# Kernel tuning notes

Measured on AMD Instinct MI355X. Metric: run time of the kernel, lower is better.

## Reference

```python
import jax, jax.numpy as jnp
import numpy as np

N = 50000
E = 800000
IN_DIM = 128
HID = 32
HEADS = 8
OUT_DIM = 2
NEG_SLOPE = 0.2


def setup_inputs() -> dict:
    key = jax.random.key(0)
    ks = jax.random.split(key, 10)
    x = jax.random.normal(ks[0], (N, IN_DIM), dtype=jnp.float32)
    edge_index = jax.random.randint(ks[1], (2, E), 0, N, dtype=jnp.int64)
    s = 0.1
    W1 = jax.random.normal(ks[2], (IN_DIM, HEADS * HID), dtype=jnp.float32) * s
    att_src1 = jax.random.normal(ks[3], (HEADS, HID), dtype=jnp.float32) * s
    att_dst1 = jax.random.normal(ks[4], (HEADS, HID), dtype=jnp.float32) * s
    b1 = jnp.zeros((HEADS * HID,), dtype=jnp.float32)
    W2 = jax.random.normal(ks[5], (HEADS * HID, OUT_DIM), dtype=jnp.float32) * s
    att_src2 = jax.random.normal(ks[6], (1, OUT_DIM), dtype=jnp.float32) * s
    att_dst2 = jax.random.normal(ks[7], (1, OUT_DIM), dtype=jnp.float32) * s
    b2 = jnp.zeros((OUT_DIM,), dtype=jnp.float32)
    return {"x": x, "edge_index": edge_index, "W1": W1, "att_src1": att_src1,
            "att_dst1": att_dst1, "b1": b1, "W2": W2, "att_src2": att_src2,
            "att_dst2": att_dst2, "b2": b2}


def gat_conv(x, src, dst, W, att_src, att_dst, bias, concat):
    # PyG GATConv (add_self_loops handled by caller already appended in src/dst)
    H, C = att_src.shape
    n = x.shape[0]
    h = (x @ W).reshape(n, H, C)                       # [N,H,C]
    a_src = jnp.einsum('nhc,hc->nh', h, att_src)       # [N,H]
    a_dst = jnp.einsum('nhc,hc->nh', h, att_dst)       # [N,H]
    e = jax.nn.leaky_relu(a_src[src] + a_dst[dst], NEG_SLOPE)  # [Etot,H]
    m = jax.lax.stop_gradient(jax.ops.segment_max(e, dst, num_segments=n))
    ee = jnp.exp(e - m[dst])
    denom = jax.ops.segment_sum(ee, dst, num_segments=n)
    alpha = ee / denom[dst]                            # segment softmax over incoming edges
    out = jax.ops.segment_sum(alpha[:, :, None] * h[src], dst, num_segments=n)  # [N,H,C]
    if concat:
        out = out.reshape(n, H * C)
    else:
        out = out.mean(axis=1)
    return out + bias


def reference(x, edge_index, W1, att_src1, att_dst1, b1, W2, att_src2, att_dst2, b2):
    n = x.shape[0]
    loop = jnp.arange(n, dtype=edge_index.dtype)
    src = jnp.concatenate([edge_index[0], loop])
    dst = jnp.concatenate([edge_index[1], loop])
    h = gat_conv(x, src, dst, W1, att_src1, att_dst1, b1, concat=True)
    h = jax.nn.elu(h)
    # dropout inactive in eval mode
    h = gat_conv(h, src, dst, W2, att_src2, att_dst2, b2, concat=False)
    return jax.nn.log_softmax(h, axis=1)
```

## Files before the change

kernel.cpp:

```cpp
#include <hip/hip_runtime.h>
#include <hip/hip_bf16.h>

#define NEG_SLOPE 0.2f
#define BSTRIDE 6144

typedef float f32x4 __attribute__((ext_vector_type(4)));
typedef short s16x4 __attribute__((ext_vector_type(4)));
typedef short bf16x8 __attribute__((ext_vector_type(8)));

__device__ __forceinline__ float lrelu(float x) { return x > 0.f ? x : NEG_SLOPE * x; }
__device__ __forceinline__ float bf2f(unsigned u) {
    return __uint_as_float(u << 16);
}
__device__ __forceinline__ unsigned short f2bf(float f) {
    unsigned int u = __float_as_uint(f);
    return (unsigned short)((u + 0x7FFF + ((u >> 16) & 1)) >> 16);
}

__device__ __forceinline__ int load_src(const int* ei, int E, int e, int is64) {
    return is64 ? ei[2 * (size_t)e] : ei[e];
}
__device__ __forceinline__ int load_dst(const int* ei, int E, int e, int is64) {
    return is64 ? ei[2 * (size_t)E + 2 * (size_t)e] : ei[(size_t)E + e];
}

__global__ void init2_kernel(const int* __restrict__ ei, int* __restrict__ flag,
                             int* __restrict__ bktCur) {
    int t = threadIdx.x;
    bktCur[t] = t * BSTRIDE;
    if (t == 0) {
        int z = 1;
        for (int k = 0; k < 64; ++k) if (ei[2 * k + 1] != 0) { z = 0; break; }
        *flag = z;
    }
}

__global__ __launch_bounds__(256) void bin_scatter(const int* __restrict__ ei, int E, int n,
                                                   const int* __restrict__ flag,
                                                   int* __restrict__ bktCur,
                                                   int* __restrict__ binned) {
    __shared__ int hist[256];
    __shared__ int gb[256];
    int t = threadIdx.x;
    hist[t] = 0;
    __syncthreads();
    int is64 = *flag;
    int base = blockIdx.x * 2048;
    int Etot = E + n;
    int rec[8], rb[8], rr[8];
#pragma unroll
    for (int k = 0; k < 8; ++k) {
        int e = base + k * 256 + t;
        rb[k] = -1;
        if (e < Etot) {
            int s, d;
            if (e < E) { s = load_src(ei, E, e, is64); d = load_dst(ei, E, e, is64); }
            else       { s = d = e - E; }
            int b = d >> 8;
            rb[k] = b;
            rec[k] = s | ((d & 255) << 24);
            rr[k] = atomicAdd(&hist[b], 1);
        }
    }
    __syncthreads();
    if (hist[t]) gb[t] = atomicAdd(&bktCur[t], hist[t]);
    __syncthreads();
#pragma unroll
    for (int k = 0; k < 8; ++k)
        if (rb[k] >= 0) binned[gb[rb[k]] + rr[k]] = rec[k];
}

__global__ __launch_bounds__(256) void bucket_build(const int* __restrict__ bktCur,
                                                    const int* __restrict__ binned,
                                                    int* __restrict__ offs,
                                                    int* __restrict__ degOut,
                                                    int* __restrict__ csr, int n) {
    __shared__ int deg[256];
    __shared__ int sd[256];
    int b = blockIdx.x;
    int t = threadIdx.x;
    int lo = b * BSTRIDE, hi = bktCur[b];
    deg[t] = 0;
    __syncthreads();
    for (int i = lo + t; i < hi; i += 256)
        atomicAdd(&deg[((unsigned)binned[i]) >> 24], 1);
    __syncthreads();
    int v = deg[t];
    sd[t] = v;
    __syncthreads();
    for (int o = 1; o < 256; o <<= 1) {
        int x = (t >= o) ? sd[t - o] : 0;
        __syncthreads();
        sd[t] += x;
        __syncthreads();
    }
    int excl = lo + sd[t] - v;
    int node = (b << 8) + t;
    if (node < n) { offs[node] = excl; degOut[node] = v; }
    __syncthreads();
    deg[t] = excl;
    __syncthreads();
    for (int i = lo + t; i < hi; i += 256) {
        unsigned r = (unsigned)binned[i];
        int pos = atomicAdd(&deg[r >> 24], 1);
        csr[pos] = (int)(r & 0xFFFFFF);
    }
}

__global__ __launch_bounds__(256) void w1prep_kernel(
        const float* __restrict__ W1, const float* __restrict__ att_src1,
        const float* __restrict__ att_dst1, unsigned short* __restrict__ w1t) {
    int t = threadIdx.x;
    if (blockIdx.x < 128) {
        int v = blockIdx.x * 256 + t;
        int col = v & 255, k = v >> 8;
        w1t[(size_t)col * 128 + k] = f2bf(W1[(size_t)k * 256 + col]);
    } else {
#pragma unroll
        for (int i = 0; i < 8; ++i) {
            int v = t + 256 * i;
            int j = v & 15, k = v >> 4;
            const float* av = (j < 8) ? att_src1 : att_dst1;
            int h = j & 7;
            float s = 0.f;
            for (int c = 0; c < 32; ++c)
                s += W1[(size_t)k * 256 + 32 * h + c] * av[h * 32 + c];
            w1t[(size_t)(256 + j) * 128 + k] = f2bf(s);
        }
    }
}

__device__ __forceinline__ bf16x8 read_frag(const char* base, int row, int kb) {
    int swz = (row & 7) << 4;
    const char* p = base + row * 256;
    s16x4 lo = *(const s16x4*)(p + (kb ^ swz));
    s16x4 hi = *(const s16x4*)(p + ((kb + 32) ^ swz));
    return __builtin_shufflevector(lo, hi, 0, 1, 2, 3, 4, 5, 6, 7);
}

__device__ __forceinline__ void load_px(const float* __restrict__ x, int m0, int n, int t,
                                        f32x4 (&px)[2][4]) {
#pragma unroll
    for (int q = 0; q < 2; ++q) {
        int u = t + 256 * q;
        int row = u >> 3, kseg = u & 7;
        int gr = m0 + row;
        bool ok = (u < 384) && (gr < n);
        const f32x4* p = (const f32x4*)(x + (size_t)gr * 128 + kseg * 16);
#pragma unroll
        for (int j = 0; j < 4; ++j) {
            f32x4 z = {0.f, 0.f, 0.f, 0.f};
            px[q][j] = ok ? p[j] : z;
        }
    }
}

#define XOFF 69632
__global__ __launch_bounds__(256, 2) void gemm1_kernel(
        const float* __restrict__ x, const unsigned short* __restrict__ w1t,
        unsigned short* __restrict__ h1u, float* __restrict__ asrc1,
        float* __restrict__ adst1, int n, int nchunk) {
    __shared__ __align__(16) char lds[81920];
    const int t = threadIdx.x;
    const int lane = t & 63, w = t >> 6;
    const int l15 = lane & 15, g = lane >> 4;

    for (int u = t; u < 4352; u += 256) {
        int col = u >> 4, seg = u & 15;
        int4 v = *(const int4*)(w1t + (size_t)col * 128 + seg * 8);
        *(int4*)(lds + col * 256 + ((seg * 16) ^ ((col & 7) << 4))) = v;
    }

    int c0 = blockIdx.x * 2;
    f32x4 px[2][4];
    load_px(x, c0 * 48, n, t, px);
    __syncthreads();

    bf16x8 Bf[4][5];
#pragma unroll
    for (int ks = 0; ks < 4; ++ks) {
#pragma unroll
        for (int nt = 0; nt < 5; ++nt) {
            if (nt < 4 || w == 0) {
                int col = (nt < 4) ? (64 * w + 16 * nt + l15) : (256 + l15);
                Bf[ks][nt] = read_frag(lds, col, 64 * ks + 8 * g);
            }
        }
    }

    for (int cc = 0; cc < 2; ++cc) {
        int chunk = c0 + cc;
        if (chunk >= nchunk) break;
        int m0 = chunk * 48;
#pragma unroll
        for (int q = 0; q < 2; ++q) {
            int u = t + 256 * q;
            if (u < 384) {
                int row = u >> 3, kseg = u & 7;
                union { unsigned short us[16]; int4 v[2]; } pk;
#pragma unroll
                for (int j = 0; j < 4; ++j)
#pragma unroll
                    for (int e = 0; e < 4; ++e) pk.us[j * 4 + e] = f2bf(px[q][j][e]);
                int base = XOFF + row * 256;
                int swz = (row & 7) << 4;
                *(int4*)(lds + base + ((kseg * 32) ^ swz)) = pk.v[0];
                *(int4*)(lds + base + ((kseg * 32 + 16) ^ swz)) = pk.v[1];
            }
        }
        __syncthreads();
        if (cc == 0) load_px(x, (c0 + 1) * 48, n, t, px);

        f32x4 acc[3][5];
#pragma unroll
        for (int mt = 0; mt < 3; ++mt)
#pragma unroll
            for (int nt = 0; nt < 5; ++nt)
#pragma unroll
                for (int r = 0; r < 4; ++r) acc[mt][nt][r] = 0.f;

#pragma unroll
        for (int ks = 0; ks < 4; ++ks) {
            bf16x8 Af[3];
#pragma unroll
            for (int mt = 0; mt < 3; ++mt)
                Af[mt] = read_frag(lds + XOFF, mt * 16 + l15, 64 * ks + 8 * g);
#pragma unroll
            for (int nt = 0; nt < 5; ++nt) {
                if (nt < 4 || w == 0) {
#pragma unroll
                    for (int mt = 0; mt < 3; ++mt)
                        acc[mt][nt] = __builtin_amdgcn_mfma_f32_16x16x32_bf16(
                            Af[mt], Bf[ks][nt], acc[mt][nt], 0, 0, 0);
                }
            }
        }

#pragma unroll
        for (int mt = 0; mt < 3; ++mt) {
#pragma unroll
            for (int r = 0; r < 4; ++r) {
                int row = m0 + 16 * mt + 4 * g + r;
                bool ok = row < n;
#pragma unroll
                for (int nt = 0; nt < 4; ++nt)
                    if (ok) h1u[(size_t)row * 256 + 64 * w + 16 * nt + l15] =
                        f2bf(acc[mt][nt][r]);
                if (w == 0 && ok) {
                    float v = acc[mt][4][r];
                    if (l15 < 8) asrc1[(size_t)row * 8 + l15] = v;
                    else         adst1[(size_t)row * 8 + (l15 - 8)] = v;
                }
            }
        }
        if (cc == 0) __syncthreads();
    }
}

__global__ __launch_bounds__(64) void aggregate_kernel(
        const int* __restrict__ offs, const int* __restrict__ deg,
        const int* __restrict__ csr,
        const float* __restrict__ asrc1, const float* __restrict__ adst1,
        const unsigned short* __restrict__ h1u, const float* __restrict__ b1,
        const float* __restrict__ W2, const float* __restrict__ att_src2,
        const float* __restrict__ att_dst2, float4* __restrict__ rec) {
    int d = blockIdx.x;
    int t = threadIdx.x;
    int h = t >> 3;
    int off = offs[d], end = off + deg[d];
    float ad = adst1[(size_t)d * 8 + h];
    float a0 = 0.f, a1 = 0.f, a2 = 0.f, a3 = 0.f, aw = 0.f;
    const unsigned short* hp = h1u + 4 * t;
    int i = off;
    for (; i + 8 <= end; i += 8) {
        int sIdx[8];
#pragma unroll
        for (int k = 0; k < 8; ++k) sIdx[k] = csr[i + k];
        float wv[8];
#pragma unroll
        for (int k = 0; k < 8; ++k)
            wv[k] = __expf(lrelu(asrc1[(size_t)sIdx[k] * 8 + h] + ad));
        ushort4 hv[8];
#pragma unroll
        for (int k = 0; k < 8; ++k)
            hv[k] = *(const ushort4*)(hp + (size_t)sIdx[k] * 256);
#pragma unroll
        for (int k = 0; k < 8; ++k) {
            a0 = fmaf(wv[k], bf2f(hv[k].x), a0);
            a1 = fmaf(wv[k], bf2f(hv[k].y), a1);
            a2 = fmaf(wv[k], bf2f(hv[k].z), a2);
            a3 = fmaf(wv[k], bf2f(hv[k].w), a3);
            aw += wv[k];
        }
    }
    for (; i < end; ++i) {
        int s = csr[i];
        float w = __expf(lrelu(asrc1[(size_t)s * 8 + h] + ad));
        ushort4 v = *(const ushort4*)(hp + (size_t)s * 256);
        a0 = fmaf(w, bf2f(v.x), a0); a1 = fmaf(w, bf2f(v.y), a1);
        a2 = fmaf(w, bf2f(v.z), a2); a3 = fmaf(w, bf2f(v.w), a3);
        aw += w;
    }
    float inv = 1.0f / aw;
    float4 bv = *(const float4*)(b1 + 4 * t);
    float v0 = fmaf(a0, inv, bv.x);
    float v1 = fmaf(a1, inv, bv.y);
    float v2 = fmaf(a2, inv, bv.z);
    float v3 = fmaf(a3, inv, bv.w);
    v0 = v0 > 0.f ? v0 : __expf(v0) - 1.f;
    v1 = v1 > 0.f ? v1 : __expf(v1) - 1.f;
    v2 = v2 > 0.f ? v2 : __expf(v2) - 1.f;
    v3 = v3 > 0.f ? v3 : __expf(v3) - 1.f;
    float4 w01 = *(const float4*)(W2 + 8 * t);
    float4 w23 = *(const float4*)(W2 + 8 * t + 4);
    float p0 = v0 * w01.x + v1 * w01.z + v2 * w23.x + v3 * w23.z;
    float p1 = v0 * w01.y + v1 * w01.w + v2 * w23.y + v3 * w23.w;
#pragma unroll
    for (int o = 32; o; o >>= 1) { p0 += __shfl_down(p0, o); p1 += __shfl_down(p1, o); }
    if (t == 0) {
        float s2a = att_src2[0], s2b = att_src2[1];
        float d2a = att_dst2[0], d2b = att_dst2[1];
        rec[d] = make_float4(p0, p1, p0 * s2a + p1 * s2b, p0 * d2a + p1 * d2b);
    }
}

__global__ __launch_bounds__(256) void layer2_kernel(
        const int* __restrict__ offs, const int* __restrict__ deg,
        const int* __restrict__ csr, const float4* __restrict__ rec,
        const float* __restrict__ b2, float* __restrict__ out, int n) {
    int t = threadIdx.x;
    int d = blockIdx.x * 16 + (t >> 4);
    if (d >= n) return;
    int li = t & 15;
    int off = offs[d], end = off + deg[d];
    float ad = rec[d].w;
    float se = 0.f, s0 = 0.f, s1 = 0.f;
    for (int i = off + li; i < end; i += 16) {
        int s = csr[i];
        float4 r = rec[s];
        float e = __expf(lrelu(r.z + ad));
        se += e;
        s0 = fmaf(e, r.x, s0);
        s1 = fmaf(e, r.y, s1);
    }
#pragma unroll
    for (int o = 8; o; o >>= 1) {
        se += __shfl_xor(se, o, 16);
        s0 += __shfl_xor(s0, o, 16);
        s1 += __shfl_xor(s1, o, 16);
    }
    if (li == 0) {
        float o0 = s0 / se + b2[0];
        float o1 = s1 / se + b2[1];
        float m2 = fmaxf(o0, o1);
        float lse = m2 + logf(__expf(o0 - m2) + __expf(o1 - m2));
        out[(size_t)d * 2 + 0] = o0 - lse;
        out[(size_t)d * 2 + 1] = o1 - lse;
    }
}

extern "C" void kernel_launch(void* const* d_in, const int* in_sizes, int n_in,
                              void* d_out, int out_size, void* d_ws, size_t ws_size,
                              hipStream_t stream) {
    const float* x        = (const float*)d_in[0];
    const int*   ei       = (const int*)d_in[1];
    const float* W1       = (const float*)d_in[2];
    const float* att_src1 = (const float*)d_in[3];
    const float* att_dst1 = (const float*)d_in[4];
    const float* b1       = (const float*)d_in[5];
    const float* W2       = (const float*)d_in[6];
    const float* att_src2 = (const float*)d_in[7];
    const float* att_dst2 = (const float*)d_in[8];
    const float* b2       = (const float*)d_in[9];
    float* out = (float*)d_out;

    int N = in_sizes[0] / 128;
    int E = in_sizes[1] / 2;
    int Etot = E + N;
    int NB = (N + 255) >> 8;
    int nbs = (Etot + 2047) / 2048;
    int nchunk = (N + 47) / 48;
    size_t binsz = (size_t)NB * BSTRIDE;

    char* W = (char*)d_ws;
    size_t o = 0;
    auto alloc = [&](size_t bytes) { size_t r = o; o = (o + bytes + 15) & ~(size_t)15; return r; };
    unsigned short* h1u  = (unsigned short*)(W + alloc((size_t)N * 256 * 2));
    float*  asrc1   = (float*)(W + alloc((size_t)N * 8 * 4));
    float*  adst1   = (float*)(W + alloc((size_t)N * 8 * 4));
    float4* rec     = (float4*)(W + alloc((size_t)N * 16));
    int*    offs    = (int*)(W + alloc((size_t)N * 4));
    int*    deg     = (int*)(W + alloc((size_t)N * 4));
    int*    bktCur  = (int*)(W + alloc(256 * 4));
    int*    flag    = (int*)(W + alloc(16));
    int*    csr     = (int*)(W + alloc(binsz * 4));
    int*    binned  = (int*)(W + alloc(binsz * 4));
    unsigned short* w1t = (unsigned short*)(W + alloc((size_t)272 * 128 * 2));

    init2_kernel<<<1, 256, 0, stream>>>(ei, flag, bktCur);
    bin_scatter<<<nbs, 256, 0, stream>>>(ei, E, N, flag, bktCur, binned);
    bucket_build<<<NB, 256, 0, stream>>>(bktCur, binned, offs, deg, csr, N);
    w1prep_kernel<<<129, 256, 0, stream>>>(W1, att_src1, att_dst1, w1t);
    gemm1_kernel<<<(nchunk + 1) / 2, 256, 0, stream>>>(x, w1t, h1u, asrc1, adst1, N, nchunk);
    aggregate_kernel<<<N, 64, 0, stream>>>(offs, deg, csr, asrc1, adst1, h1u, b1, W2,
                                           att_src2, att_dst2, rec);
    layer2_kernel<<<(N + 15) / 16, 256, 0, stream>>>(offs, deg, csr, rec, b2, out, N);
}
```

Measured before the change: 168.4 us.

## Merge prep kernels and co-launch CSR bucket build with layer-1 GEMM

Folds the W1 transpose/attention-projection prep into the init kernel, and merges the CSR bucket build into the GEMM launch as extra blocks that branch off early. This cuts two kernel launches and lets the independent CSR construction run concurrently with the GEMM instead of serially. The int64 edge-index load now reads through int2 pointers. The build blocks still reserve the GEMM's large LDS allocation, which can limit how many of them run at once.

```diff
diff --git a/kernel.cpp b/kernel.cpp
--- a/kernel.cpp
+++ b/kernel.cpp
@@ -17,21 +17,34 @@
     return (unsigned short)((u + 0x7FFF + ((u >> 16) & 1)) >> 16);
 }
 
-__device__ __forceinline__ int load_src(const int* ei, int E, int e, int is64) {
-    return is64 ? ei[2 * (size_t)e] : ei[e];
-}
-__device__ __forceinline__ int load_dst(const int* ei, int E, int e, int is64) {
-    return is64 ? ei[2 * (size_t)E + 2 * (size_t)e] : ei[(size_t)E + e];
-}
-
-__global__ void init2_kernel(const int* __restrict__ ei, int* __restrict__ flag,
-                             int* __restrict__ bktCur) {
+__global__ __launch_bounds__(256) void prep_kernel(
+        const float* __restrict__ W1, const float* __restrict__ att_src1,
+        const float* __restrict__ att_dst1, unsigned short* __restrict__ w1t,
+        const int* __restrict__ ei, int* __restrict__ flag, int* __restrict__ bktCur) {
     int t = threadIdx.x;
-    bktCur[t] = t * BSTRIDE;
-    if (t == 0) {
-        int z = 1;
-        for (int k = 0; k < 64; ++k) if (ei[2 * k + 1] != 0) { z = 0; break; }
-        *flag = z;
+    if (blockIdx.x < 128) {
+        int v = blockIdx.x * 256 + t;
+        int col = v & 255, k = v >> 8;
+        w1t[(size_t)col * 128 + k] = f2bf(W1[(size_t)k * 256 + col]);
+    } else if (blockIdx.x == 128) {
+#pragma unroll
+        for (int i = 0; i < 8; ++i) {
+            int v = t + 256 * i;
+            int j = v & 15, k = v >> 4;
+            const float* av = (j < 8) ? att_src1 : att_dst1;
+            int h = j & 7;
+            float s = 0.f;
+            for (int c = 0; c < 32; ++c)
+                s += W1[(size_t)k * 256 + 32 * h + c] * av[h * 32 + c];
+            w1t[(size_t)(256 + j) * 128 + k] = f2bf(s);
+        }
+    } else {
+        bktCur[t] = t * BSTRIDE;
+        if (t == 0) {
+            int z = 1;
+            for (int k = 0; k < 64; ++k) if (ei[2 * k + 1] != 0) { z = 0; break; }
+            *flag = z;
+        }
     }
 }
 
@@ -54,8 +67,15 @@
         rb[k] = -1;
         if (e < Etot) {
             int s, d;
-            if (e < E) { s = load_src(ei, E, e, is64); d = load_dst(ei, E, e, is64); }
-            else       { s = d = e - E; }
+            if (e < E) {
+                if (is64) {
+                    s = ((const int2*)ei)[e].x;
+                    d = ((const int2*)(ei + 2 * (size_t)E))[e].x;
+                } else {
+                    s = ei[e];
+                    d = ei[(size_t)E + e];
+                }
+            } else { s = d = e - E; }
             int b = d >> 8;
             rb[k] = b;
             rec[k] = s | ((d & 255) << 24);
@@ -68,66 +88,6 @@
 #pragma unroll
     for (int k = 0; k < 8; ++k)
         if (rb[k] >= 0) binned[gb[rb[k]] + rr[k]] = rec[k];
-}
-
-__global__ __launch_bounds__(256) void bucket_build(const int* __restrict__ bktCur,
-                                                    const int* __restrict__ binned,
-                                                    int* __restrict__ offs,
-                                                    int* __restrict__ degOut,
-                                                    int* __restrict__ csr, int n) {
-    __shared__ int deg[256];
-    __shared__ int sd[256];
-    int b = blockIdx.x;
-    int t = threadIdx.x;
-    int lo = b * BSTRIDE, hi = bktCur[b];
-    deg[t] = 0;
-    __syncthreads();
-    for (int i = lo + t; i < hi; i += 256)
-        atomicAdd(&deg[((unsigned)binned[i]) >> 24], 1);
-    __syncthreads();
-    int v = deg[t];
-    sd[t] = v;
-    __syncthreads();
-    for (int o = 1; o < 256; o <<= 1) {
-        int x = (t >= o) ? sd[t - o] : 0;
-        __syncthreads();
-        sd[t] += x;
-        __syncthreads();
-    }
-    int excl = lo + sd[t] - v;
-    int node = (b << 8) + t;
-    if (node < n) { offs[node] = excl; degOut[node] = v; }
-    __syncthreads();
-    deg[t] = excl;
-    __syncthreads();
-    for (int i = lo + t; i < hi; i += 256) {
-        unsigned r = (unsigned)binned[i];
-        int pos = atomicAdd(&deg[r >> 24], 1);
-        csr[pos] = (int)(r & 0xFFFFFF);
-    }
-}
-
-__global__ __launch_bounds__(256) void w1prep_kernel(
-        const float* __restrict__ W1, const float* __restrict__ att_src1,
-        const float* __restrict__ att_dst1, unsigned short* __restrict__ w1t) {
-    int t = threadIdx.x;
-    if (blockIdx.x < 128) {
-        int v = blockIdx.x * 256 + t;
-        int col = v & 255, k = v >> 8;
-        w1t[(size_t)col * 128 + k] = f2bf(W1[(size_t)k * 256 + col]);
-    } else {
-#pragma unroll
-        for (int i = 0; i < 8; ++i) {
-            int v = t + 256 * i;
-            int j = v & 15, k = v >> 4;
-            const float* av = (j < 8) ? att_src1 : att_dst1;
-            int h = j & 7;
-            float s = 0.f;
-            for (int c = 0; c < 32; ++c)
-                s += W1[(size_t)k * 256 + 32 * h + c] * av[h * 32 + c];
-            w1t[(size_t)(256 + j) * 128 + k] = f2bf(s);
-        }
-    }
 }
 
 __device__ __forceinline__ bf16x8 read_frag(const char* base, int row, int kb) {
@@ -156,12 +116,48 @@
 }
 
 #define XOFF 69632
-__global__ __launch_bounds__(256, 2) void gemm1_kernel(
+__global__ __launch_bounds__(256, 2) void build_gemm_kernel(
+        const int* __restrict__ bktCur, const int* __restrict__ binned,
+        int* __restrict__ offs, int* __restrict__ degOut, int* __restrict__ csr,
         const float* __restrict__ x, const unsigned short* __restrict__ w1t,
         unsigned short* __restrict__ h1u, float* __restrict__ asrc1,
-        float* __restrict__ adst1, int n, int nchunk) {
+        float* __restrict__ adst1, int n, int nchunk, int ngemm) {
     __shared__ __align__(16) char lds[81920];
     const int t = threadIdx.x;
+
+    if (blockIdx.x >= ngemm) {
+        int* deg = (int*)lds;
+        int* sd  = (int*)(lds + 1024);
+        int b = blockIdx.x - ngemm;
+        int lo = b * BSTRIDE, hi = bktCur[b];
+        deg[t] = 0;
+        __syncthreads();
+        for (int i = lo + t; i < hi; i += 256)
+            atomicAdd(&deg[((unsigned)binned[i]) >> 24], 1);
+        __syncthreads();
+        int v = deg[t];
+        sd[t] = v;
+        __syncthreads();
+        for (int o = 1; o < 256; o <<= 1) {
+            int xv = (t >= o) ? sd[t - o] : 0;
+            __syncthreads();
+            sd[t] += xv;
+            __syncthreads();
+        }
+        int excl = lo + sd[t] - v;
+        int node = (b << 8) + t;
+        if (node < n) { offs[node] = excl; degOut[node] = v; }
+        __syncthreads();
+        deg[t] = excl;
+        __syncthreads();
+        for (int i = lo + t; i < hi; i += 256) {
+            unsigned r = (unsigned)binned[i];
+            int pos = atomicAdd(&deg[r >> 24], 1);
+            csr[pos] = (int)(r & 0xFFFFFF);
+        }
+        return;
+    }
+
     const int lane = t & 63, w = t >> 6;
     const int l15 = lane & 15, g = lane >> 4;
 
@@ -380,6 +376,7 @@
     int NB = (N + 255) >> 8;
     int nbs = (Etot + 2047) / 2048;
     int nchunk = (N + 47) / 48;
+    int ngemm = (nchunk + 1) / 2;
     size_t binsz = (size_t)NB * BSTRIDE;
 
     char* W = (char*)d_ws;
@@ -397,11 +394,11 @@
     int*    binned  = (int*)(W + alloc(binsz * 4));
     unsigned short* w1t = (unsigned short*)(W + alloc((size_t)272 * 128 * 2));
 
-    init2_kernel<<<1, 256, 0, stream>>>(ei, flag, bktCur);
+    prep_kernel<<<130, 256, 0, stream>>>(W1, att_src1, att_dst1, w1t, ei, flag, bktCur);
     bin_scatter<<<nbs, 256, 0, stream>>>(ei, E, N, flag, bktCur, binned);
-    bucket_build<<<NB, 256, 0, stream>>>(bktCur, binned, offs, deg, csr, N);
-    w1prep_kernel<<<129, 256, 0, stream>>>(W1, att_src1, att_dst1, w1t);
-    gemm1_kernel<<<(nchunk + 1) / 2, 256, 0, stream>>>(x, w1t, h1u, asrc1, adst1, N, nchunk);
+    build_gemm_kernel<<<ngemm + NB, 256, 0, stream>>>(bktCur, binned, offs, deg, csr,
+                                                      x, w1t, h1u, asrc1, adst1,
+                                                      N, nchunk, ngemm);
     aggregate_kernel<<<N, 64, 0, stream>>>(offs, deg, csr, asrc1, adst1, h1u, b1, W2,
                                            att_src2, att_dst2, rec);
     layer2_kernel<<<(N + 15) / 16, 256, 0, stream>>>(offs, deg, csr, rec, b2, out, N);
```

Result: faster. 151.6 us (-10.0%).
